# Kernel optimization log

Measured on AMD Instinct MI355X. Metric: run time of the kernel, lower is better.

The kernel has to match this reference:

```python
import jax, jax.numpy as jnp
import numpy as np

jax.config.update("jax_enable_x64", True)

# Module hyperparameters (see init_kwargs)
INPUT_DIM = 128
EMBED_DIM = 64
CHUNK = 8            # chunk_size
BITS = 8             # bits_per_chunk
NREP = 2             # num_rep
NCHUNKS = EMBED_DIM // CHUNK  # 8
ARRAY = 262144       # array_size = memory_size / num_rep
MEM = ARRAY * NREP   # hashed_weights length
BATCH = 524288
PRIME = 2038074743


def _generate_sparse_srp(rng, n, d):
    # weighted_values / generateSparseSRP from the torch module
    vals = np.array([1.0, -1.0, 0.0])
    bins = np.add.accumulate(np.array([0.1667, 0.1667, 0.6666]))
    return vals[np.digitize(rng.random_sample(n * d), bins)].astype(np.float32).reshape(n, d)


def setup_inputs() -> dict:
    key = jax.random.key(0)
    k1, k2 = jax.random.split(key)
    x = jax.random.normal(k1, (BATCH, INPUT_DIM), dtype=jnp.float32)
    hashed_weights = jax.random.normal(k2, (MEM,), dtype=jnp.float32) * 0.02
    rng = np.random.RandomState(1024)
    lsh = _generate_sparse_srp(rng, INPUT_DIM, NREP * NCHUNKS * BITS).reshape(
        INPUT_DIM, NREP, NCHUNKS * BITS)
    random_numbers = np.concatenate(
        [np.array([PRIME]), rng.randint(0, PRIME, (50,))]).astype(np.int64)
    return {
        "x": x,
        "hashed_weights": hashed_weights,
        "lsh_matrix": jnp.asarray(lsh),
        "random_numbers": jnp.asarray(random_numbers),
    }


def _hashed_indices(x, lsh_matrix, random_numbers):
    """SRP hash -> bucket id per (rep, chunk) -> universal hash -> chunk start."""
    B = x.shape[0]
    # sparse random projection: [B, R, C*bits]
    proj = jnp.einsum('bi,irk->brk', x, lsh_matrix)
    bits = (proj > 0).astype(jnp.int64).reshape(B, NREP, NCHUNKS, BITS)
    powers = jnp.int64(1) << jnp.arange(BITS, dtype=jnp.int64)
    srp = jnp.sum(bits * powers, axis=-1)  # [B, R, C] in [0, 2^BITS)
    P = random_numbers[0]
    a, b, c0 = random_numbers[1], random_numbers[2], random_numbers[3]
    chunk_ids = jnp.arange(NCHUNKS, dtype=jnp.int64)  # broadcast over [B, R, C]
    # universal hash of (bucket, chunk) -> start of a contiguous chunk in the array
    loc = ((a * srp + b * chunk_ids + c0) % P) % (ARRAY - CHUNK + 1)  # [B, R, C]
    rep_off = (jnp.arange(NREP, dtype=jnp.int64) * ARRAY)[None, :, None, None]
    idx = rep_off + loc[..., None] + jnp.arange(CHUNK, dtype=jnp.int64)  # [B,R,C,cs]
    return idx.reshape(B, NREP, EMBED_DIM)


def reference(x, hashed_weights, lsh_matrix, random_numbers):
    hashed_idx = _hashed_indices(x, lsh_matrix, random_numbers)  # [B, R, E] int64
    # gather chunks from the shared hashed table and average over reps
    output = jnp.mean(hashed_weights[hashed_idx], axis=1)  # [B, E]
    return hashed_idx, output
```

## Files before the change

kernel.cpp:

```cpp
#include <hip/hip_runtime.h>
#include <stdint.h>

typedef __attribute__((ext_vector_type(8))) short short8;
typedef __attribute__((ext_vector_type(4))) float f32x4;

constexpr int      BATCH    = 524288;
constexpr int      ARRAY_SZ = 262144;
constexpr uint64_t PRIME    = 2038074743ull;
constexpr uint32_t RANGE    = 262137u;
constexpr int      NMT      = BATCH / 16;
constexpr float    EPS      = 8e-5f;

__device__ __forceinline__ void load_hash_consts(const void* rnd_raw,
                                                 uint64_t& HA, uint64_t& HB, uint64_t& HC0)
{
    const uint64_t first8 = *reinterpret_cast<const uint64_t*>(rnd_raw);
    if (first8 == PRIME) {
        const long long* r64 = reinterpret_cast<const long long*>(rnd_raw);
        HA = (uint64_t)r64[1]; HB = (uint64_t)r64[2]; HC0 = (uint64_t)r64[3];
    } else {
        const int* r32 = reinterpret_cast<const int*>(rnd_raw);
        HA  = (uint64_t)(uint32_t)r32[1];
        HB  = (uint64_t)(uint32_t)r32[2];
        HC0 = (uint64_t)(uint32_t)r32[3];
    }
}

__global__ __launch_bounds__(256, 2)
void lma_srp(const float* __restrict__ x,
             const float* __restrict__ lsh,
             const void* __restrict__ rnd_raw,
             uint32_t* __restrict__ rec_out)
{
    __shared__ unsigned short T[128 * 128];

    const int tid  = threadIdx.x;
    const int lane = tid & 63;
    const int wid  = __builtin_amdgcn_readfirstlane(tid >> 6);

    for (int it = 0; it < 16; ++it) {
        const int flat4 = it * 256 + tid;
        const int i  = flat4 >> 5;
        const int n4 = (flat4 & 31) << 2;
        const f32x4 v = *reinterpret_cast<const f32x4*>(lsh + i * 128 + n4);
#pragma unroll
        for (int d = 0; d < 4; ++d) {
            const int n = n4 + d;
            T[n * 128 + (((i >> 3) ^ (n & 15)) << 3) + (i & 7)] =
                (unsigned short)(__float_as_uint(v[d]) >> 16);
        }
    }
    __syncthreads();

    const int r    = lane & 15;
    const int g    = lane >> 4;
    const int e    = lane >> 2;
    const int c4   = lane & 3;
    const int hf   = c4 & 1;
    const int npar = c4 >> 1;
    const int shb  = 16 * (e >> 2) + 8 * hf;
    const int sel  = e & 3;
    const bool s0 = (sel == 0), s1 = (sel == 1), s2 = (sel == 2);

    const int mt0 = blockIdx.x * 4 + wid;
    f32x4 xp0, xp1, xp2, xp3, xp4, xp5, xp6, xp7;
    {
        const float* xn = x + (size_t)mt0 * 16 * 128 + r * 128 + g * 8;
        xp0 = *reinterpret_cast<const f32x4*>(xn);
        xp1 = *reinterpret_cast<const f32x4*>(xn + 4);
        xp2 = *reinterpret_cast<const f32x4*>(xn + 32);
        xp3 = *reinterpret_cast<const f32x4*>(xn + 36);
        xp4 = *reinterpret_cast<const f32x4*>(xn + 64);
        xp5 = *reinterpret_cast<const f32x4*>(xn + 68);
        xp6 = *reinterpret_cast<const f32x4*>(xn + 96);
        xp7 = *reinterpret_cast<const f32x4*>(xn + 100);
    }

#pragma unroll 1
    for (int mt = mt0; mt < NMT; mt += 8192) {
        const int Mb = mt * 16;

        f32x4 acc[8];
#pragma unroll
        for (int n8 = 0; n8 < 8; ++n8) acc[n8] = (f32x4)(0.0f);
        float asum = 0.0f;

#pragma unroll
        for (int ks = 0; ks < 4; ++ks) {
            const f32x4 xa = (ks == 0) ? xp0 : (ks == 1) ? xp2 : (ks == 2) ? xp4 : xp6;
            const f32x4 xc = (ks == 0) ? xp1 : (ks == 1) ? xp3 : (ks == 2) ? xp5 : xp7;
            float xs[8] = {xa[0], xa[1], xa[2], xa[3], xc[0], xc[1], xc[2], xc[3]};
#pragma unroll
            for (int j = 0; j < 8; ++j) asum += fabsf(xs[j]);

            union { uint32_t u[4]; short8 v; } Ahi, Ami;
#pragma unroll
            for (int p = 0; p < 4; ++p) {
                const uint32_t b0 = __float_as_uint(xs[2 * p]);
                const uint32_t b1 = __float_as_uint(xs[2 * p + 1]);
                const uint32_t h0 = b0 & 0xFFFF0000u, h1 = b1 & 0xFFFF0000u;
                const float    t0 = xs[2 * p] - __uint_as_float(h0);
                const float    t1 = xs[2 * p + 1] - __uint_as_float(h1);
                const uint32_t m0 = __float_as_uint(t0) & 0xFFFF0000u;
                const uint32_t m1 = __float_as_uint(t1) & 0xFFFF0000u;
                Ahi.u[p] = h1 | (h0 >> 16);
                Ami.u[p] = m1 | (m0 >> 16);
            }
#pragma unroll
            for (int n8 = 0; n8 < 8; ++n8) {
                const short8 bf = *reinterpret_cast<const short8*>(
                    &T[(n8 * 16 + r) * 128 + (((ks * 4 + g) ^ r) << 3)]);
                acc[n8] = __builtin_amdgcn_mfma_f32_16x16x32_bf16(Ahi.v, bf, acc[n8], 0, 0, 0);
                acc[n8] = __builtin_amdgcn_mfma_f32_16x16x32_bf16(Ami.v, bf, acc[n8], 0, 0, 0);
            }
        }

        {
            const int mtn = (mt + 8192 < NMT) ? mt + 8192 : mt;
            const float* xn = x + (size_t)mtn * 16 * 128 + r * 128 + g * 8;
            xp0 = *reinterpret_cast<const f32x4*>(xn);
            xp1 = *reinterpret_cast<const f32x4*>(xn + 4);
            xp2 = *reinterpret_cast<const f32x4*>(xn + 32);
            xp3 = *reinterpret_cast<const f32x4*>(xn + 36);
            xp4 = *reinterpret_cast<const f32x4*>(xn + 64);
            xp5 = *reinterpret_cast<const f32x4*>(xn + 68);
            xp6 = *reinterpret_cast<const f32x4*>(xn + 96);
            xp7 = *reinterpret_cast<const f32x4*>(xn + 100);
        }
        __builtin_amdgcn_sched_barrier(0);

        asum += __shfl_xor(asum, 16);
        asum += __shfl_xor(asum, 32);
        float bndr[4];
#pragma unroll
        for (int reg = 0; reg < 4; ++reg)
            bndr[reg] = __shfl(asum, (lane >> 4) * 4 + reg) * EPS;

        uint32_t wsrp = 0, wflg = 0;
#pragma unroll
        for (int n8 = 0; n8 < 8; ++n8) {
            const unsigned long long sb0 = __ballot(acc[n8][0] > 0.0f);
            const unsigned long long sb1 = __ballot(acc[n8][1] > 0.0f);
            const unsigned long long sb2 = __ballot(acc[n8][2] > 0.0f);
            const unsigned long long sb3 = __ballot(acc[n8][3] > 0.0f);
            const unsigned long long fb0 = __ballot(fabsf(acc[n8][0]) <= bndr[0]);
            const unsigned long long fb1 = __ballot(fabsf(acc[n8][1]) <= bndr[1]);
            const unsigned long long fb2 = __ballot(fabsf(acc[n8][2]) <= bndr[2]);
            const unsigned long long fb3 = __ballot(fabsf(acc[n8][3]) <= bndr[3]);
            const unsigned long long sbx = s0 ? sb0 : s1 ? sb1 : s2 ? sb2 : sb3;
            const unsigned long long fbx = s0 ? fb0 : s1 ? fb1 : s2 ? fb2 : fb3;
            if ((n8 & 1) == npar) {
                const int mshift = ((n8 - npar) >> 1) * 8;
                wsrp |= (uint32_t)((sbx >> shb) & 0xffull) << mshift;
                wflg |= (uint32_t)((fbx >> shb) & 0xffull) << mshift;
            }
        }

        const size_t eg = (size_t)(Mb + e);
        if (wflg) {
            const float* xr = x + eg * 128;
            for (uint32_t fb = wflg; fb; fb &= fb - 1) {
                const int bit = __builtin_ctz(fb);
                const int m   = bit >> 3;
                const int j   = bit & 7;
                const int k   = (c4 + 4 * m) * 8 + j;
                float s = 0.0f;
#pragma unroll 4
                for (int i8 = 0; i8 < 16; ++i8) {
                    const uint4 tb = *reinterpret_cast<const uint4*>(
                        &T[k * 128 + ((i8 ^ (k & 15)) << 3)]);
                    const f32x4 xA = *reinterpret_cast<const f32x4*>(xr + i8 * 8);
                    const f32x4 xB = *reinterpret_cast<const f32x4*>(xr + i8 * 8 + 4);
                    const uint32_t tu[4] = {tb.x, tb.y, tb.z, tb.w};
                    s = __builtin_fmaf(xA[0], __uint_as_float(tu[0] << 16), s);
                    s = __builtin_fmaf(xA[1], __uint_as_float(tu[0] & 0xFFFF0000u), s);
                    s = __builtin_fmaf(xA[2], __uint_as_float(tu[1] << 16), s);
                    s = __builtin_fmaf(xA[3], __uint_as_float(tu[1] & 0xFFFF0000u), s);
                    s = __builtin_fmaf(xB[0], __uint_as_float(tu[2] << 16), s);
                    s = __builtin_fmaf(xB[1], __uint_as_float(tu[2] & 0xFFFF0000u), s);
                    s = __builtin_fmaf(xB[2], __uint_as_float(tu[3] << 16), s);
                    s = __builtin_fmaf(xB[3], __uint_as_float(tu[3] & 0xFFFF0000u), s);
                }
                wsrp = (wsrp & ~(1u << bit)) | ((s > 0.0f) ? (1u << bit) : 0u);
            }
        }
        rec_out[eg * 4 + c4] = wsrp;
    }
}

__global__ __launch_bounds__(256, 8)
void lma_emit(const float* __restrict__ hw,
              const uint32_t* __restrict__ rec,
              const void* __restrict__ rnd_raw,
              float* __restrict__ out_idx,
              float* __restrict__ out_val)
{
    uint64_t HA, HB, HC0;
    load_hash_consts(rnd_raw, HA, HB, HC0);

    const int gtid = blockIdx.x * 256 + threadIdx.x;
    const int e    = gtid >> 4;
    const int cc   = gtid & 15;
    const int cch  = cc & 7;
    const int rep  = cc >> 3;

    const uint4 rv = *reinterpret_cast<const uint4*>(rec + (size_t)e * 4);
    const int compo = cc & 3;
    const uint32_t dw = (compo == 0) ? rv.x : (compo == 1) ? rv.y
                      : (compo == 2) ? rv.z : rv.w;
    const uint32_t srp = (dw >> (8 * (cc >> 2))) & 0xFFu;

    const uint64_t hh  = (HA * (uint64_t)srp + HB * (uint64_t)cch + HC0) % PRIME;
    const uint32_t loc = (uint32_t)hh % RANGE + (rep ? (uint32_t)ARRAY_SZ : 0u);

    const float f0 = (float)loc;
    float* oi = out_idx + (size_t)e * 128 + cc * 8;
    *reinterpret_cast<f32x4*>(oi)     = (f32x4){f0, f0 + 1.f, f0 + 2.f, f0 + 3.f};
    *reinterpret_cast<f32x4*>(oi + 4) = (f32x4){f0 + 4.f, f0 + 5.f, f0 + 6.f, f0 + 7.f};

    float wv[8];
#pragma unroll
    for (int j = 0; j < 8; ++j) wv[j] = hw[loc + j];

    float v[8];
#pragma unroll
    for (int j = 0; j < 8; ++j)
        v[j] = (wv[j] + __shfl_xor(wv[j], 8)) * 0.5f;

    if (rep == 0) {
        float* ov = out_val + (size_t)e * 64 + cc * 8;
        *reinterpret_cast<f32x4*>(ov)     = (f32x4){v[0], v[1], v[2], v[3]};
        *reinterpret_cast<f32x4*>(ov + 4) = (f32x4){v[4], v[5], v[6], v[7]};
    }
}

extern "C" void kernel_launch(void* const* d_in, const int* in_sizes, int n_in,
                              void* d_out, int out_size, void* d_ws, size_t ws_size,
                              hipStream_t stream) {
    const float* x   = (const float*)d_in[0];
    const float* hw  = (const float*)d_in[1];
    const float* lsh = (const float*)d_in[2];
    const void*  rnd = (const void*)d_in[3];

    float*    out_idx = (float*)d_out;
    float*    out_val = out_idx + (size_t)BATCH * 128;
    uint32_t* recbuf  = (uint32_t*)d_ws;

    lma_srp <<<2048, 256, 0, stream>>>(x, lsh, rnd, recbuf);
    lma_emit<<<BATCH * 16 / 256, 256, 0, stream>>>(hw, recbuf, rnd, out_idx, out_val);
}
```

Baseline: 251.6 us.

## Replace persistent SRP loop with one 16-row tile per wave grid

```diff
diff --git a/kernel.cpp b/kernel.cpp
--- a/kernel.cpp
+++ b/kernel.cpp
@@ -27,10 +27,9 @@
 }
 
 __global__ __launch_bounds__(256, 2)
-void lma_srp(const float* __restrict__ x,
-             const float* __restrict__ lsh,
-             const void* __restrict__ rnd_raw,
-             uint32_t* __restrict__ rec_out)
+void lma_srp1(const float* __restrict__ x,
+              const float* __restrict__ lsh,
+              uint32_t* __restrict__ rec_out)
 {
     __shared__ unsigned short T[128 * 128];
 
@@ -62,130 +61,108 @@
     const int sel  = e & 3;
     const bool s0 = (sel == 0), s1 = (sel == 1), s2 = (sel == 2);
 
-    const int mt0 = blockIdx.x * 4 + wid;
-    f32x4 xp0, xp1, xp2, xp3, xp4, xp5, xp6, xp7;
-    {
-        const float* xn = x + (size_t)mt0 * 16 * 128 + r * 128 + g * 8;
-        xp0 = *reinterpret_cast<const f32x4*>(xn);
-        xp1 = *reinterpret_cast<const f32x4*>(xn + 4);
-        xp2 = *reinterpret_cast<const f32x4*>(xn + 32);
-        xp3 = *reinterpret_cast<const f32x4*>(xn + 36);
-        xp4 = *reinterpret_cast<const f32x4*>(xn + 64);
-        xp5 = *reinterpret_cast<const f32x4*>(xn + 68);
-        xp6 = *reinterpret_cast<const f32x4*>(xn + 96);
-        xp7 = *reinterpret_cast<const f32x4*>(xn + 100);
-    }
-
-#pragma unroll 1
-    for (int mt = mt0; mt < NMT; mt += 8192) {
-        const int Mb = mt * 16;
-
-        f32x4 acc[8];
-#pragma unroll
-        for (int n8 = 0; n8 < 8; ++n8) acc[n8] = (f32x4)(0.0f);
-        float asum = 0.0f;
-
-#pragma unroll
-        for (int ks = 0; ks < 4; ++ks) {
-            const f32x4 xa = (ks == 0) ? xp0 : (ks == 1) ? xp2 : (ks == 2) ? xp4 : xp6;
-            const f32x4 xc = (ks == 0) ? xp1 : (ks == 1) ? xp3 : (ks == 2) ? xp5 : xp7;
-            float xs[8] = {xa[0], xa[1], xa[2], xa[3], xc[0], xc[1], xc[2], xc[3]};
-#pragma unroll
-            for (int j = 0; j < 8; ++j) asum += fabsf(xs[j]);
-
-            union { uint32_t u[4]; short8 v; } Ahi, Ami;
-#pragma unroll
-            for (int p = 0; p < 4; ++p) {
-                const uint32_t b0 = __float_as_uint(xs[2 * p]);
-                const uint32_t b1 = __float_as_uint(xs[2 * p + 1]);
-                const uint32_t h0 = b0 & 0xFFFF0000u, h1 = b1 & 0xFFFF0000u;
-                const float    t0 = xs[2 * p] - __uint_as_float(h0);
-                const float    t1 = xs[2 * p + 1] - __uint_as_float(h1);
-                const uint32_t m0 = __float_as_uint(t0) & 0xFFFF0000u;
-                const uint32_t m1 = __float_as_uint(t1) & 0xFFFF0000u;
-                Ahi.u[p] = h1 | (h0 >> 16);
-                Ami.u[p] = m1 | (m0 >> 16);
+    const int mt = blockIdx.x * 4 + wid;
+    const float* xn = x + (size_t)mt * 16 * 128 + r * 128 + g * 8;
+    const f32x4 xp0 = *reinterpret_cast<const f32x4*>(xn);
+    const f32x4 xp1 = *reinterpret_cast<const f32x4*>(xn + 4);
+    const f32x4 xp2 = *reinterpret_cast<const f32x4*>(xn + 32);
+    const f32x4 xp3 = *reinterpret_cast<const f32x4*>(xn + 36);
+    const f32x4 xp4 = *reinterpret_cast<const f32x4*>(xn + 64);
+    const f32x4 xp5 = *reinterpret_cast<const f32x4*>(xn + 68);
+    const f32x4 xp6 = *reinterpret_cast<const f32x4*>(xn + 96);
+    const f32x4 xp7 = *reinterpret_cast<const f32x4*>(xn + 100);
+
+    f32x4 acc[8];
+#pragma unroll
+    for (int n8 = 0; n8 < 8; ++n8) acc[n8] = (f32x4)(0.0f);
+    float asum = 0.0f;
+
+#pragma unroll
+    for (int ks = 0; ks < 4; ++ks) {
+        const f32x4 xa = (ks == 0) ? xp0 : (ks == 1) ? xp2 : (ks == 2) ? xp4 : xp6;
+        const f32x4 xc = (ks == 0) ? xp1 : (ks == 1) ? xp3 : (ks == 2) ? xp5 : xp7;
+        float xs[8] = {xa[0], xa[1], xa[2], xa[3], xc[0], xc[1], xc[2], xc[3]};
+#pragma unroll
+        for (int j = 0; j < 8; ++j) asum += fabsf(xs[j]);
+
+        union { uint32_t u[4]; short8 v; } Ahi, Ami;
+#pragma unroll
+        for (int p = 0; p < 4; ++p) {
+            const uint32_t b0 = __float_as_uint(xs[2 * p]);
+            const uint32_t b1 = __float_as_uint(xs[2 * p + 1]);
+            const uint32_t h0 = b0 & 0xFFFF0000u, h1 = b1 & 0xFFFF0000u;
+            const float    t0 = xs[2 * p] - __uint_as_float(h0);
+            const float    t1 = xs[2 * p + 1] - __uint_as_float(h1);
+            const uint32_t m0 = __float_as_uint(t0) & 0xFFFF0000u;
+            const uint32_t m1 = __float_as_uint(t1) & 0xFFFF0000u;
+            Ahi.u[p] = h1 | (h0 >> 16);
+            Ami.u[p] = m1 | (m0 >> 16);
+        }
+#pragma unroll
+        for (int n8 = 0; n8 < 8; ++n8) {
+            const short8 bf = *reinterpret_cast<const short8*>(
+                &T[(n8 * 16 + r) * 128 + (((ks * 4 + g) ^ r) << 3)]);
+            acc[n8] = __builtin_amdgcn_mfma_f32_16x16x32_bf16(Ahi.v, bf, acc[n8], 0, 0, 0);
+            acc[n8] = __builtin_amdgcn_mfma_f32_16x16x32_bf16(Ami.v, bf, acc[n8], 0, 0, 0);
+        }
+    }
+
+    asum += __shfl_xor(asum, 16);
+    asum += __shfl_xor(asum, 32);
+    float bndr[4];
+#pragma unroll
+    for (int reg = 0; reg < 4; ++reg)
+        bndr[reg] = __shfl(asum, (lane >> 4) * 4 + reg) * EPS;
+
+    uint32_t wsrp = 0, wflg = 0;
+#pragma unroll
+    for (int n8 = 0; n8 < 8; ++n8) {
+        const unsigned long long sb0 = __ballot(acc[n8][0] > 0.0f);
+        const unsigned long long sb1 = __ballot(acc[n8][1] > 0.0f);
+        const unsigned long long sb2 = __ballot(acc[n8][2] > 0.0f);
+        const unsigned long long sb3 = __ballot(acc[n8][3] > 0.0f);
+        const unsigned long long fb0 = __ballot(fabsf(acc[n8][0]) <= bndr[0]);
+        const unsigned long long fb1 = __ballot(fabsf(acc[n8][1]) <= bndr[1]);
+        const unsigned long long fb2 = __ballot(fabsf(acc[n8][2]) <= bndr[2]);
+        const unsigned long long fb3 = __ballot(fabsf(acc[n8][3]) <= bndr[3]);
+        const unsigned long long sbx = s0 ? sb0 : s1 ? sb1 : s2 ? sb2 : sb3;
+        const unsigned long long fbx = s0 ? fb0 : s1 ? fb1 : s2 ? fb2 : fb3;
+        if ((n8 & 1) == npar) {
+            const int mshift = ((n8 - npar) >> 1) * 8;
+            wsrp |= (uint32_t)((sbx >> shb) & 0xffull) << mshift;
+            wflg |= (uint32_t)((fbx >> shb) & 0xffull) << mshift;
+        }
+    }
+
+    const size_t eg = (size_t)(mt * 16 + e);
+    if (wflg) {
+        const float* xr = x + eg * 128;
+        for (uint32_t fb = wflg; fb; fb &= fb - 1) {
+            const int bit = __builtin_ctz(fb);
+            const int m   = bit >> 3;
+            const int j   = bit & 7;
+            const int k   = (c4 + 4 * m) * 8 + j;
+            float s = 0.0f;
+#pragma unroll 4
+            for (int i8 = 0; i8 < 16; ++i8) {
+                const uint4 tb = *reinterpret_cast<const uint4*>(
+                    &T[k * 128 + ((i8 ^ (k & 15)) << 3)]);
+                const f32x4 xA = *reinterpret_cast<const f32x4*>(xr + i8 * 8);
+                const f32x4 xB = *reinterpret_cast<const f32x4*>(xr + i8 * 8 + 4);
+                const uint32_t tu[4] = {tb.x, tb.y, tb.z, tb.w};
+                s = __builtin_fmaf(xA[0], __uint_as_float(tu[0] << 16), s);
+                s = __builtin_fmaf(xA[1], __uint_as_float(tu[0] & 0xFFFF0000u), s);
+                s = __builtin_fmaf(xA[2], __uint_as_float(tu[1] << 16), s);
+                s = __builtin_fmaf(xA[3], __uint_as_float(tu[1] & 0xFFFF0000u), s);
+                s = __builtin_fmaf(xB[0], __uint_as_float(tu[2] << 16), s);
+                s = __builtin_fmaf(xB[1], __uint_as_float(tu[2] & 0xFFFF0000u), s);
+                s = __builtin_fmaf(xB[2], __uint_as_float(tu[3] << 16), s);
+                s = __builtin_fmaf(xB[3], __uint_as_float(tu[3] & 0xFFFF0000u), s);
             }
-#pragma unroll
-            for (int n8 = 0; n8 < 8; ++n8) {
-                const short8 bf = *reinterpret_cast<const short8*>(
-                    &T[(n8 * 16 + r) * 128 + (((ks * 4 + g) ^ r) << 3)]);
-                acc[n8] = __builtin_amdgcn_mfma_f32_16x16x32_bf16(Ahi.v, bf, acc[n8], 0, 0, 0);
-                acc[n8] = __builtin_amdgcn_mfma_f32_16x16x32_bf16(Ami.v, bf, acc[n8], 0, 0, 0);
-            }
-        }
-
-        {
-            const int mtn = (mt + 8192 < NMT) ? mt + 8192 : mt;
-            const float* xn = x + (size_t)mtn * 16 * 128 + r * 128 + g * 8;
-            xp0 = *reinterpret_cast<const f32x4*>(xn);
-            xp1 = *reinterpret_cast<const f32x4*>(xn + 4);
-            xp2 = *reinterpret_cast<const f32x4*>(xn + 32);
-            xp3 = *reinterpret_cast<const f32x4*>(xn + 36);
-            xp4 = *reinterpret_cast<const f32x4*>(xn + 64);
-            xp5 = *reinterpret_cast<const f32x4*>(xn + 68);
-            xp6 = *reinterpret_cast<const f32x4*>(xn + 96);
-            xp7 = *reinterpret_cast<const f32x4*>(xn + 100);
-        }
-        __builtin_amdgcn_sched_barrier(0);
-
-        asum += __shfl_xor(asum, 16);
-        asum += __shfl_xor(asum, 32);
-        float bndr[4];
-#pragma unroll
-        for (int reg = 0; reg < 4; ++reg)
-            bndr[reg] = __shfl(asum, (lane >> 4) * 4 + reg) * EPS;
-
-        uint32_t wsrp = 0, wflg = 0;
-#pragma unroll
-        for (int n8 = 0; n8 < 8; ++n8) {
-            const unsigned long long sb0 = __ballot(acc[n8][0] > 0.0f);
-            const unsigned long long sb1 = __ballot(acc[n8][1] > 0.0f);
-            const unsigned long long sb2 = __ballot(acc[n8][2] > 0.0f);
-            const unsigned long long sb3 = __ballot(acc[n8][3] > 0.0f);
-            const unsigned long long fb0 = __ballot(fabsf(acc[n8][0]) <= bndr[0]);
-            const unsigned long long fb1 = __ballot(fabsf(acc[n8][1]) <= bndr[1]);
-            const unsigned long long fb2 = __ballot(fabsf(acc[n8][2]) <= bndr[2]);
-            const unsigned long long fb3 = __ballot(fabsf(acc[n8][3]) <= bndr[3]);
-            const unsigned long long sbx = s0 ? sb0 : s1 ? sb1 : s2 ? sb2 : sb3;
-            const unsigned long long fbx = s0 ? fb0 : s1 ? fb1 : s2 ? fb2 : fb3;
-            if ((n8 & 1) == npar) {
-                const int mshift = ((n8 - npar) >> 1) * 8;
-                wsrp |= (uint32_t)((sbx >> shb) & 0xffull) << mshift;
-                wflg |= (uint32_t)((fbx >> shb) & 0xffull) << mshift;
-            }
-        }
-
-        const size_t eg = (size_t)(Mb + e);
-        if (wflg) {
-            const float* xr = x + eg * 128;
-            for (uint32_t fb = wflg; fb; fb &= fb - 1) {
-                const int bit = __builtin_ctz(fb);
-                const int m   = bit >> 3;
-                const int j   = bit & 7;
-                const int k   = (c4 + 4 * m) * 8 + j;
-                float s = 0.0f;
-#pragma unroll 4
-                for (int i8 = 0; i8 < 16; ++i8) {
-                    const uint4 tb = *reinterpret_cast<const uint4*>(
-                        &T[k * 128 + ((i8 ^ (k & 15)) << 3)]);
-                    const f32x4 xA = *reinterpret_cast<const f32x4*>(xr + i8 * 8);
-                    const f32x4 xB = *reinterpret_cast<const f32x4*>(xr + i8 * 8 + 4);
-                    const uint32_t tu[4] = {tb.x, tb.y, tb.z, tb.w};
-                    s = __builtin_fmaf(xA[0], __uint_as_float(tu[0] << 16), s);
-                    s = __builtin_fmaf(xA[1], __uint_as_float(tu[0] & 0xFFFF0000u), s);
-                    s = __builtin_fmaf(xA[2], __uint_as_float(tu[1] << 16), s);
-                    s = __builtin_fmaf(xA[3], __uint_as_float(tu[1] & 0xFFFF0000u), s);
-                    s = __builtin_fmaf(xB[0], __uint_as_float(tu[2] << 16), s);
-                    s = __builtin_fmaf(xB[1], __uint_as_float(tu[2] & 0xFFFF0000u), s);
-                    s = __builtin_fmaf(xB[2], __uint_as_float(tu[3] << 16), s);
-                    s = __builtin_fmaf(xB[3], __uint_as_float(tu[3] & 0xFFFF0000u), s);
-                }
-                wsrp = (wsrp & ~(1u << bit)) | ((s > 0.0f) ? (1u << bit) : 0u);
-            }
-        }
-        rec_out[eg * 4 + c4] = wsrp;
-    }
+            wsrp = (wsrp & ~(1u << bit)) | ((s > 0.0f) ? (1u << bit) : 0u);
+        }
+    }
+    rec_out[eg * 4 + c4] = wsrp;
 }
 
 __global__ __launch_bounds__(256, 8)
@@ -246,6 +223,6 @@
     float*    out_val = out_idx + (size_t)BATCH * 128;
     uint32_t* recbuf  = (uint32_t*)d_ws;
 
-    lma_srp <<<2048, 256, 0, stream>>>(x, lsh, rnd, recbuf);
+    lma_srp1<<<NMT / 4, 256, 0, stream>>>(x, lsh, recbuf);
     lma_emit<<<BATCH * 16 / 256, 256, 0, stream>>>(hw, recbuf, rnd, out_idx, out_val);
 }
```

New measurement: 285.7 us. 1.14x slower.

## Precompute hash location and weight tables for all bucket/chunk pairs

Applied to the files above, without the earlier changes.

```diff
diff --git a/kernel.cpp b/kernel.cpp
--- a/kernel.cpp
+++ b/kernel.cpp
@@ -26,10 +26,30 @@
     }
 }
 
+__global__ __launch_bounds__(256, 1)
+void lma_tab(const float* __restrict__ hw,
+             const void* __restrict__ rnd_raw,
+             uint32_t* __restrict__ locTab,
+             float* __restrict__ wTab)
+{
+    uint64_t HA, HB, HC0;
+    load_hash_consts(rnd_raw, HA, HB, HC0);
+
+    const int t   = blockIdx.x * 256 + threadIdx.x;
+    const int srp = t & 255;
+    const int cc  = t >> 8;
+    const int cch = cc & 7;
+
+    const uint64_t hh  = (HA * (uint64_t)srp + HB * (uint64_t)cch + HC0) % PRIME;
+    const uint32_t loc = (uint32_t)hh % RANGE + ((cc >> 3) ? (uint32_t)ARRAY_SZ : 0u);
+    locTab[t] = loc;
+#pragma unroll
+    for (int j = 0; j < 8; ++j) wTab[t * 8 + j] = hw[loc + j];
+}
+
 __global__ __launch_bounds__(256, 2)
 void lma_srp(const float* __restrict__ x,
              const float* __restrict__ lsh,
-             const void* __restrict__ rnd_raw,
              uint32_t* __restrict__ rec_out)
 {
     __shared__ unsigned short T[128 * 128];
@@ -189,19 +209,15 @@
 }
 
 __global__ __launch_bounds__(256, 8)
-void lma_emit(const float* __restrict__ hw,
-              const uint32_t* __restrict__ rec,
-              const void* __restrict__ rnd_raw,
+void lma_emit(const uint32_t* __restrict__ rec,
+              const uint32_t* __restrict__ locTab,
+              const float* __restrict__ wTab,
               float* __restrict__ out_idx,
               float* __restrict__ out_val)
 {
-    uint64_t HA, HB, HC0;
-    load_hash_consts(rnd_raw, HA, HB, HC0);
-
     const int gtid = blockIdx.x * 256 + threadIdx.x;
     const int e    = gtid >> 4;
     const int cc   = gtid & 15;
-    const int cch  = cc & 7;
     const int rep  = cc >> 3;
 
     const uint4 rv = *reinterpret_cast<const uint4*>(rec + (size_t)e * 4);
@@ -210,22 +226,23 @@
                       : (compo == 2) ? rv.z : rv.w;
     const uint32_t srp = (dw >> (8 * (cc >> 2))) & 0xFFu;
 
-    const uint64_t hh  = (HA * (uint64_t)srp + HB * (uint64_t)cch + HC0) % PRIME;
-    const uint32_t loc = (uint32_t)hh % RANGE + (rep ? (uint32_t)ARRAY_SZ : 0u);
+    const int      ti  = (cc << 8) | (int)srp;
+    const uint32_t loc = locTab[ti];
 
     const float f0 = (float)loc;
     float* oi = out_idx + (size_t)e * 128 + cc * 8;
     *reinterpret_cast<f32x4*>(oi)     = (f32x4){f0, f0 + 1.f, f0 + 2.f, f0 + 3.f};
     *reinterpret_cast<f32x4*>(oi + 4) = (f32x4){f0 + 4.f, f0 + 5.f, f0 + 6.f, f0 + 7.f};
 
-    float wv[8];
-#pragma unroll
-    for (int j = 0; j < 8; ++j) wv[j] = hw[loc + j];
+    const f32x4 w0 = *reinterpret_cast<const f32x4*>(wTab + (size_t)ti * 8);
+    const f32x4 w1 = *reinterpret_cast<const f32x4*>(wTab + (size_t)ti * 8 + 4);
 
     float v[8];
 #pragma unroll
-    for (int j = 0; j < 8; ++j)
-        v[j] = (wv[j] + __shfl_xor(wv[j], 8)) * 0.5f;
+    for (int j = 0; j < 4; ++j) {
+        v[j]     = (w0[j] + __shfl_xor(w0[j], 8)) * 0.5f;
+        v[4 + j] = (w1[j] + __shfl_xor(w1[j], 8)) * 0.5f;
+    }
 
     if (rep == 0) {
         float* ov = out_val + (size_t)e * 64 + cc * 8;
@@ -242,10 +259,16 @@
     const float* lsh = (const float*)d_in[2];
     const void*  rnd = (const void*)d_in[3];
 
-    float*    out_idx = (float*)d_out;
-    float*    out_val = out_idx + (size_t)BATCH * 128;
-    uint32_t* recbuf  = (uint32_t*)d_ws;
-
-    lma_srp <<<2048, 256, 0, stream>>>(x, lsh, rnd, recbuf);
-    lma_emit<<<BATCH * 16 / 256, 256, 0, stream>>>(hw, recbuf, rnd, out_idx, out_val);
-}
+    float* out_idx = (float*)d_out;
+    float* out_val = out_idx + (size_t)BATCH * 128;
+
+    uint8_t*  ws      = (uint8_t*)d_ws;
+    uint32_t* recbuf  = (uint32_t*)ws;
+    uint32_t* locTab  = (uint32_t*)(ws + (size_t)BATCH * 16);
+    float*    wTab    = (float*)(ws + (size_t)BATCH * 16 + 4096 * 4);
+
+    lma_tab <<<16, 256, 0, stream>>>(hw, rnd, locTab, wTab);
+    lma_srp <<<2048, 256, 0, stream>>>(x, lsh, recbuf);
+    lma_emit<<<BATCH * 16 / 256, 256, 0, stream>>>(recbuf, locTab, wTab,
+                                                   out_idx, out_val);
+}
```

New measurement: 241.8 us. -3.9%, faster.
